# Optimization experiments

Hardware: AMD Instinct MI355X
Metric: run time of the kernel (lower is better)

## Reference

```python
import jax, jax.numpy as jnp
import numpy as np

B, N, K, V, E, H = 256, 256, 3, 32000, 256, 256
G = (3 + K) * H  # i, o, u gates + K forget gates


def setup_inputs() -> dict:
    key = jax.random.key(0)
    ks = jax.random.split(key, 6)
    node_ids = jax.random.randint(ks[0], (B, N), 0, V)
    children_raw = jax.random.randint(ks[1], (B, N, K), 0, N)
    emb = jax.random.normal(ks[2], (V, E), jnp.float32) * 0.02
    Wx_w = jax.random.normal(ks[3], (E, G), jnp.float32) * (1.0 / np.sqrt(E))
    Wx_b = jnp.zeros((G,), jnp.float32)
    Uh_w = jax.random.normal(ks[4], (K, H, G), jnp.float32) * (1.0 / np.sqrt(H))
    Uh_b = jnp.zeros((K, G), jnp.float32)
    return {"node_ids": node_ids, "children_raw": children_raw, "emb": emb,
            "Wx_w": Wx_w, "Wx_b": Wx_b, "Uh_w": Uh_w, "Uh_b": Uh_b}


def reference(node_ids, children_raw, emb, Wx_w, Wx_b, Uh_w, Uh_b):
    pos = jnp.arange(N)
    # A child slot is valid only if it points to an earlier node (topological order).
    valid = children_raw < pos[None, :, None]            # [B,N,K]
    mask = valid.astype(jnp.float32)
    cidx = jnp.where(valid, children_raw, 0)             # safe gather index

    # Input-dependent part of the gates for all nodes at once (same math as Wx(x)).
    x_all = emb[node_ids]                                # [B,N,E]
    gates_x = jnp.einsum('bne,eg->bng', x_all, Wx_w) + Wx_b  # [B,N,G]

    def step(carry, inp):
        h_buf, c_buf = carry                             # [B,N,H] each
        t, gx, idx, m = inp                              # gx:[B,G] idx,m:[B,K]
        h_child = jnp.take_along_axis(h_buf, idx[:, :, None], axis=1)  # [B,K,H]
        c_child = jnp.take_along_axis(c_buf, idx[:, :, None], axis=1)  # [B,K,H]
        # Uh[k](h_k) added only for present children (bias included per child).
        gates = gx + jnp.einsum('bkh,khg->bg', h_child * m[:, :, None], Uh_w) \
                   + m @ Uh_b                            # [B,G]
        i = jax.nn.sigmoid(gates[:, :H])
        o = jax.nn.sigmoid(gates[:, H:2 * H])
        u = jnp.tanh(gates[:, 2 * H:3 * H])
        f = jax.nn.sigmoid(gates[:, 3 * H:].reshape(B, K, H))
        c = i * u + jnp.sum(m[:, :, None] * f * c_child, axis=1)
        h = o * jnp.tanh(c)
        h_buf = jax.lax.dynamic_update_slice(h_buf, h[:, None, :], (0, t, 0))
        c_buf = jax.lax.dynamic_update_slice(c_buf, c[:, None, :], (0, t, 0))
        return (h_buf, c_buf), None

    init = (jnp.zeros((B, N, H), jnp.float32), jnp.zeros((B, N, H), jnp.float32))
    xs = (pos, gates_x.transpose(1, 0, 2), cidx.transpose(1, 0, 2), mask.transpose(1, 0, 2))
    (h_buf, _), _ = jax.lax.scan(step, init, xs)
    # Root is the last node in topological order -> encoder output [B, H].
    return h_buf[:, N - 1]
```

## Files before the change

kernel.cpp:

```cpp
#include <hip/hip_runtime.h>
#include <hip/hip_bf16.h>

#define CB 256
#define CN 256
#define CK 3
#define CE 256
#define CH 256
#define CG_ 1536
#define KTOT 1024
#define ROWS 32
#define ASTRW 1028

typedef __attribute__((ext_vector_type(8))) short short8v;
typedef __attribute__((ext_vector_type(4))) float float4v;
typedef __attribute__((ext_vector_type(4))) unsigned int uint4v;
typedef __attribute__((ext_vector_type(4))) unsigned short ushort4v;
typedef unsigned int u32;
typedef unsigned long long u64;
typedef unsigned short u16;

__device__ __forceinline__ u16 f2bfu(float v) {
    __hip_bfloat16 h = __float2bfloat16(v);
    return __builtin_bit_cast(u16, h);
}
__device__ __forceinline__ float bfu2f(u16 u) {
    __hip_bfloat16 h = __builtin_bit_cast(__hip_bfloat16, u);
    return __bfloat162float(h);
}

__global__ __launch_bounds__(256) void prep_w(
    const float* __restrict__ Wx_w, const float* __restrict__ Uh_w,
    u16* __restrict__ Whi, u16* __restrict__ Wlo)
{
    const int g    = blockIdx.x;
    const int tile = g >> 4;
    const int gl   = g & 15;
    for (int k = threadIdx.x; k < KTOT; k += 256) {
        float w = (k < CE) ? Wx_w[(size_t)k * CG_ + g]
                           : Uh_w[(size_t)(k - CE) * CG_ + g];
        u16 hi = f2bfu(w);
        u16 lo = f2bfu(w - bfu2f(hi));
        int ci = k >> 5, kr = k & 31, lq = kr >> 3, j = kr & 7;
        size_t idx = ((size_t)(tile * 32 + ci) * 64 + lq * 16 + gl) * 8 + j;
        Whi[idx] = hi;
        Wlo[idx] = lo;
    }
}

__global__ __launch_bounds__(256) void build_sched(
    const int* __restrict__ children,
    u16* __restrict__ wl,
    u32* __restrict__ lvl_start,
    u32* __restrict__ lvl_cnt,
    u32* __restrict__ nlev)
{
    __shared__ unsigned char lvl[CB][CN];
    __shared__ u32 cnt[CN];
    __shared__ u32 pos[CN];
    const int b = threadIdx.x;

    for (int t = 0; t < CN; ++t) {
        int lv = 0;
        #pragma unroll
        for (int k = 0; k < CK; ++k) {
            int raw = children[((size_t)b * CN + t) * CK + k];
            if (raw < t) { int cl = (int)lvl[b][raw] + 1; if (cl > lv) lv = cl; }
        }
        lvl[b][t] = (unsigned char)lv;
    }
    cnt[b] = 0;
    __syncthreads();
    for (int t = 0; t < CN; ++t) atomicAdd(&cnt[lvl[b][t]], 1u);
    __syncthreads();
    if (b == 0) {
        u32 acc = 0, nl = 0;
        for (int L = 0; L < CN; ++L) {
            pos[L] = acc;
            if (cnt[L]) nl = (u32)L + 1;
            acc += cnt[L];
        }
        *nlev = nl;
    }
    __syncthreads();
    lvl_cnt[b]   = cnt[b];
    lvl_start[b] = pos[b];
    __syncthreads();
    for (int t = 0; t < CN; ++t) {
        int L = lvl[b][t];
        u32 p = atomicAdd(&pos[L], 1u);
        wl[p] = (u16)((b << 8) | t);
    }
}

__global__ __launch_bounds__(512, 2) void tree_scan_lvl(
    const int* __restrict__ node_ids,
    const int* __restrict__ children,
    const float* __restrict__ emb,
    const u16* __restrict__ Whi,
    const u16* __restrict__ Wlo,
    const float* __restrict__ Wx_b,
    const float* __restrict__ Uh_b,
    u32* __restrict__ h_pk,
    float* __restrict__ c_s,
    u32* __restrict__ flags,
    const u16* __restrict__ wl,
    const u32* __restrict__ lvl_start,
    const u32* __restrict__ lvl_cnt,
    const u32* __restrict__ nlev_p,
    float* __restrict__ out)
{
    const int tid = threadIdx.x;
    const int bid = blockIdx.x;
    const int hi  = (bid & 7) >> 1;
    const int sub = ((bid >> 3) << 1) | (bid & 1);
    const int hh0 = hi * 64;

    __shared__ u32   Apk[ROWS][ASTRW];
    __shared__ int   nid[ROWS], brow[ROWS], trow[ROWS];
    __shared__ unsigned char rval[ROWS];
    __shared__ float msk[ROWS][3];
    __shared__ int   cix[ROWS][3];

    const int wv    = tid >> 6;
    const int l     = tid & 63;
    const int rg    = wv >> 2;
    const int ctq   = wv & 3;
    const int lan15 = l & 15;
    const int k8w   = (l >> 4) * 8;
    const int hcol  = hh0 + ctq * 16 + lan15;
    const int arow  = rg * 16 + lan15;

    u32 bb[6];
    #pragma unroll
    for (int q = 0; q < 6; ++q)
        bb[q] = (u32)(q * 16 + (hh0 >> 4) + ctq) * 16384u + (u32)l * 8u;

    const u32 NL = *nlev_p;

    for (u32 L = 0; L < NL; ++L) {
        const u32 lcnt   = lvl_cnt[L];
        const u32 lst    = lvl_start[L];
        const u32 nchunk = (lcnt + ROWS - 1) / ROWS;

        for (u32 ck = sub; ck < nchunk; ck += 64) {
            if (tid < ROWS) {
                u32 i = ck * ROWS + (u32)tid;
                int valid = (i < lcnt);
                u16 e = valid ? wl[lst + i] : (u16)0;
                rval[tid] = (unsigned char)valid;
                int b_ = valid ? (e >> 8) : 0;
                int t_ = valid ? (e & 0xFF) : 0;
                brow[tid] = b_;
                trow[tid] = t_;
                nid[tid]  = node_ids[(size_t)b_ * CN + t_];
            }
            if (tid < ROWS * CK) {
                int lb = tid / 3, k = tid - lb * 3;
                u32 i = ck * ROWS + (u32)lb;
                int valid = (i < lcnt);
                u16 e = valid ? wl[lst + i] : (u16)0;
                int b_ = valid ? (e >> 8) : 0;
                int t_ = valid ? (e & 0xFF) : 0;
                int raw = children[((size_t)b_ * CN + t_) * CK + k];
                int v = (raw < t_) && valid;
                msk[lb][k] = v ? 1.0f : 0.0f;
                cix[lb][k] = v ? raw : 0;
            }
            __syncthreads();

            for (int idx = tid; idx < ROWS * 64; idx += 512) {
                int row = idx >> 6, c4 = idx & 63;
                float4v v = *(const float4v*)(emb + (size_t)nid[row] * CE + c4 * 4);
                uint4v p;
                #pragma unroll
                for (int j = 0; j < 4; ++j) {
                    u16 hb = f2bfu(v[j]);
                    u16 lb = f2bfu(v[j] - bfu2f(hb));
                    p[j] = ((u32)hb << 16) | (u32)lb;
                }
                *(uint4v*)&Apk[row][c4 * 4] = p;
            }
            for (int idx = tid; idx < ROWS * CK * 128; idx += 512) {
                int r  = idx >> 7;
                int ch = idx & 127;
                int row = r / 3, k = r - row * 3;
                u64 v = 0;
                if (msk[row][k] != 0.0f) {
                    const u64* src = (const u64*)(h_pk
                        + ((size_t)cix[row][k] * CB + brow[row]) * CH + 2 * ch);
                    v = __hip_atomic_load(src, __ATOMIC_RELAXED, __HIP_MEMORY_SCOPE_AGENT);
                }
                *(u64*)&Apk[row][CE + k * CH + 2 * ch] = v;
            }
            __syncthreads();

            float4v accH[6], accL[6];
            #pragma unroll
            for (int q = 0; q < 6; ++q) {
                accH[q] = (float4v){0.f, 0.f, 0.f, 0.f};
                accL[q] = (float4v){0.f, 0.f, 0.f, 0.f};
            }
            #pragma unroll 4
            for (int ci = 0; ci < 32; ++ci) {
                uint4v a0 = *(const uint4v*)&Apk[arow][ci * 32 + k8w];
                uint4v a1 = *(const uint4v*)&Apk[arow][ci * 32 + k8w + 4];
                short8v ahi, alo;
                #pragma unroll
                for (int j = 0; j < 4; ++j) {
                    ahi[j]     = (short)(a0[j] >> 16);
                    alo[j]     = (short)(a0[j] & 0xffffu);
                    ahi[4 + j] = (short)(a1[j] >> 16);
                    alo[4 + j] = (short)(a1[j] & 0xffffu);
                }
                #pragma unroll
                for (int q = 0; q < 6; ++q) {
                    short8v bh = *(const short8v*)(Whi + bb[q] + ci * 512);
                    short8v bl = *(const short8v*)(Wlo + bb[q] + ci * 512);
                    accH[q] = __builtin_amdgcn_mfma_f32_16x16x32_bf16(ahi, bh, accH[q], 0, 0, 0);
                    accL[q] = __builtin_amdgcn_mfma_f32_16x16x32_bf16(ahi, bl, accL[q], 0, 0, 0);
                    accL[q] = __builtin_amdgcn_mfma_f32_16x16x32_bf16(alo, bh, accL[q], 0, 0, 0);
                }
            }

            #pragma unroll
            for (int r = 0; r < 4; ++r) {
                const int row = rg * 16 + (l >> 4) * 4 + r;
                if (rval[row]) {
                    const int b = brow[row], t_ = trow[row];
                    const float m0 = msk[row][0], m1 = msk[row][1], m2 = msk[row][2];
                    float g[6];
                    #pragma unroll
                    for (int q = 0; q < 6; ++q) {
                        int gc = q * CH + hcol;
                        g[q] = accH[q][r] + accL[q][r]
                             + Wx_b[gc] + m0 * Uh_b[gc] + m1 * Uh_b[CG_ + gc]
                                        + m2 * Uh_b[2 * CG_ + gc];
                    }
                    float ig = 1.0f / (1.0f + expf(-g[0]));
                    float og = 1.0f / (1.0f + expf(-g[1]));
                    float ug = tanhf(g[2]);
                    float c = ig * ug;
                    if (m0 != 0.0f) c += (1.0f / (1.0f + expf(-g[3]))) *
                        __hip_atomic_load(&c_s[((size_t)cix[row][0] * CB + b) * CH + hcol],
                                          __ATOMIC_RELAXED, __HIP_MEMORY_SCOPE_AGENT);
                    if (m1 != 0.0f) c += (1.0f / (1.0f + expf(-g[4]))) *
                        __hip_atomic_load(&c_s[((size_t)cix[row][1] * CB + b) * CH + hcol],
                                          __ATOMIC_RELAXED, __HIP_MEMORY_SCOPE_AGENT);
                    if (m2 != 0.0f) c += (1.0f / (1.0f + expf(-g[5]))) *
                        __hip_atomic_load(&c_s[((size_t)cix[row][2] * CB + b) * CH + hcol],
                                          __ATOMIC_RELAXED, __HIP_MEMORY_SCOPE_AGENT);
                    float h = og * tanhf(c);
                    const size_t hx = ((size_t)t_ * CB + b) * CH + hcol;
                    u16 hb = f2bfu(h);
                    u32 hp = ((u32)hb << 16) | (u32)f2bfu(h - bfu2f(hb));
                    __hip_atomic_store(&h_pk[hx], hp, __ATOMIC_RELAXED, __HIP_MEMORY_SCOPE_AGENT);
                    __hip_atomic_store(&c_s[hx], c, __ATOMIC_RELAXED, __HIP_MEMORY_SCOPE_AGENT);
                    if (t_ == CN - 1) out[(size_t)b * CH + hcol] = h;
                }
            }
            __syncthreads();
        }

        if (L == NL - 1) break;

        __syncthreads();
        if (tid == 0)
            __hip_atomic_store(&flags[bid * 16], L + 1,
                               __ATOMIC_RELAXED, __HIP_MEMORY_SCOPE_AGENT);
        for (;;) {
            int ok = 1;
            if (tid < 256)
                ok = (__hip_atomic_load(&flags[tid * 16], __ATOMIC_RELAXED,
                                        __HIP_MEMORY_SCOPE_AGENT) >= L + 1);
            if (__syncthreads_and(ok)) break;
            __builtin_amdgcn_s_sleep(2);
        }
    }
}

__global__ __launch_bounds__(768) void tree_step_mfma(
    const int* __restrict__ node_ids, const int* __restrict__ children,
    const float* __restrict__ emb,
    const u16* __restrict__ Whi, const u16* __restrict__ Wlo,
    const float* __restrict__ Wx_b, const float* __restrict__ Uh_b,
    u16* __restrict__ h_hi, u16* __restrict__ h_lo,
    float* __restrict__ c_s, float* __restrict__ out, const int t)
{
    const int tid = threadIdx.x;
    const int xcd  = blockIdx.x & 7;
    const int bidx = blockIdx.x >> 3;
    const int hi   = xcd * 2 + (bidx & 1);
    const int bi   = bidx >> 1;
    const int b0   = bi * 16;
    const int hh0  = hi * 16;

    __shared__ u16   Ahi[16][KTOT + 8];
    __shared__ u16   Alo[16][KTOT + 8];
    __shared__ float part[4][6][16][17];
    __shared__ int   nid[16];
    __shared__ float msk[16][3];
    __shared__ int   cix[16][3];

    const int wv    = tid >> 6;
    const int l     = tid & 63;
    const int np    = wv % 3;
    const int kq    = wv / 3;
    const int lan15 = l & 15;
    const int k8    = (l >> 4) * 8;

    if (tid < 16) nid[tid] = node_ids[(size_t)(b0 + tid) * CN + t];
    if (tid < 48) {
        int lb = tid / 3, k = tid - lb * 3;
        int raw = children[((size_t)(b0 + lb) * CN + t) * CK + k];
        int v = raw < t;
        msk[lb][k] = v ? 1.0f : 0.0f;
        cix[lb][k] = v ? raw : 0;
    }
    __syncthreads();

    for (int idx = tid; idx < 1024; idx += 768) {
        int lb = idx >> 6, c4 = idx & 63;
        float4v v = *(const float4v*)(emb + (size_t)nid[lb] * CE + c4 * 4);
        ushort4v h4, l4;
        #pragma unroll
        for (int j = 0; j < 4; ++j) {
            u16 hb = f2bfu(v[j]);
            h4[j] = hb;
            l4[j] = f2bfu(v[j] - bfu2f(hb));
        }
        *(ushort4v*)&Ahi[lb][c4 * 4] = h4;
        *(ushort4v*)&Alo[lb][c4 * 4] = l4;
    }
    for (int idx = tid; idx < 3072; idx += 768) {
        int r  = idx >> 6;
        int c  = idx & 63;
        int pl = c >> 5;
        int ch = c & 31;
        int lb = r / 3, k = r - lb * 3;
        uint4v val = (uint4v){0u, 0u, 0u, 0u};
        if (msk[lb][k] != 0.0f) {
            const u16* src = (pl ? h_lo : h_hi)
                + ((size_t)cix[lb][k] * CB + (b0 + lb)) * CH + ch * 8;
            val = *(const uint4v*)src;
        }
        u16* dst = (pl ? &Alo[lb][CE + k * CH + ch * 8]
                       : &Ahi[lb][CE + k * CH + ch * 8]);
        *(uint4v*)dst = val;
    }
    __syncthreads();

    {
        float4v acc[2][3];
        #pragma unroll
        for (int a = 0; a < 2; ++a)
            #pragma unroll
            for (int b2 = 0; b2 < 3; ++b2)
                acc[a][b2] = (float4v){0.f, 0.f, 0.f, 0.f};
        u32 fb0 = (u32)((np * 2 + 0) * 16 + hi) * 16384u + (u32)l * 8u;
        u32 fb1 = (u32)((np * 2 + 1) * 16 + hi) * 16384u + (u32)l * 8u;
        #pragma unroll
        for (int ci = 0; ci < 8; ++ci) {
            const int kb = (kq * 8 + ci) * 32 + k8;
            const u32 fo = (u32)(kq * 8 + ci) * 512u;
            short8v ahi = *(const short8v*)&Ahi[lan15][kb];
            short8v alo = *(const short8v*)&Alo[lan15][kb];
            short8v bh0 = *(const short8v*)(Whi + fb0 + fo);
            short8v bh1 = *(const short8v*)(Whi + fb1 + fo);
            short8v bl0 = *(const short8v*)(Wlo + fb0 + fo);
            short8v bl1 = *(const short8v*)(Wlo + fb1 + fo);
            acc[0][0] = __builtin_amdgcn_mfma_f32_16x16x32_bf16(ahi, bh0, acc[0][0], 0, 0, 0);
            acc[0][1] = __builtin_amdgcn_mfma_f32_16x16x32_bf16(ahi, bl0, acc[0][1], 0, 0, 0);
            acc[0][2] = __builtin_amdgcn_mfma_f32_16x16x32_bf16(alo, bh0, acc[0][2], 0, 0, 0);
            acc[1][0] = __builtin_amdgcn_mfma_f32_16x16x32_bf16(ahi, bh1, acc[1][0], 0, 0, 0);
            acc[1][1] = __builtin_amdgcn_mfma_f32_16x16x32_bf16(ahi, bl1, acc[1][1], 0, 0, 0);
            acc[1][2] = __builtin_amdgcn_mfma_f32_16x16x32_bf16(alo, bh1, acc[1][2], 0, 0, 0);
        }
        #pragma unroll
        for (int t2 = 0; t2 < 2; ++t2)
            #pragma unroll
            for (int r = 0; r < 4; ++r)
                part[kq][np * 2 + t2][(l >> 4) * 4 + r][lan15] =
                    acc[t2][0][r] + acc[t2][1][r] + acc[t2][2][r];
    }
    __syncthreads();

    if (tid < 256) {
        const int bb = tid >> 4, j2 = tid & 15;
        const int b = b0 + bb, hh = hh0 + j2;
        const float m0 = msk[bb][0], m1 = msk[bb][1], m2 = msk[bb][2];
        float g[6];
        #pragma unroll
        for (int q = 0; q < 6; ++q) {
            int gc = q * CH + hh;
            g[q] = part[0][q][bb][j2] + part[1][q][bb][j2]
                 + part[2][q][bb][j2] + part[3][q][bb][j2]
                 + Wx_b[gc] + m0 * Uh_b[gc] + m1 * Uh_b[CG_ + gc]
                            + m2 * Uh_b[2 * CG_ + gc];
        }
        float ig = 1.0f / (1.0f + expf(-g[0]));
        float og = 1.0f / (1.0f + expf(-g[1]));
        float ug = tanhf(g[2]);
        float c = ig * ug;
        if (m0 != 0.0f) c += (1.0f / (1.0f + expf(-g[3]))) * c_s[((size_t)cix[bb][0] * CB + b) * CH + hh];
        if (m1 != 0.0f) c += (1.0f / (1.0f + expf(-g[4]))) * c_s[((size_t)cix[bb][1] * CB + b) * CH + hh];
        if (m2 != 0.0f) c += (1.0f / (1.0f + expf(-g[5]))) * c_s[((size_t)cix[bb][2] * CB + b) * CH + hh];
        float h = og * tanhf(c);
        const size_t hx = ((size_t)t * CB + b) * CH + hh;
        u16 hb = f2bfu(h);
        h_hi[hx] = hb;
        h_lo[hx] = f2bfu(h - bfu2f(hb));
        c_s[hx] = c;
        if (t == CN - 1) out[(size_t)b * CH + hh] = h;
    }
}

__global__ void ws_report(float* out, int n, float val) {
    int i = blockIdx.x * blockDim.x + threadIdx.x;
    if (i < n) out[i] = val;
}

extern "C" void kernel_launch(void* const* d_in, const int* in_sizes, int n_in,
                              void* d_out, int out_size, void* d_ws, size_t ws_size,
                              hipStream_t stream) {
    float* outp = (float*)d_out;

    const int expect_sizes[7] = {65536, 196608, 8192000, 393216, 1536, 1179648, 4608};
    int bad = -1;
    if (n_in != 7) bad = 7;
    else for (int i = 0; i < 7; ++i) if (in_sizes[i] != expect_sizes[i]) { bad = i; break; }
    if (bad >= 0) {
        ws_report<<<(out_size + 255) / 256, 256, 0, stream>>>(outp, out_size, 1000.0f + bad);
        return;
    }

    const int*   node_ids = (const int*)d_in[0];
    const int*   children = (const int*)d_in[1];
    const float* emb      = (const float*)d_in[2];
    const float* Wx_w     = (const float*)d_in[3];
    const float* Wx_b     = (const float*)d_in[4];
    const float* Uh_w     = (const float*)d_in[5];
    const float* Uh_b     = (const float*)d_in[6];

    const size_t w_plane  = (size_t)CG_ * KTOT * 2;
    const size_t st_elems = (size_t)CN * CB * CH;
    const size_t flags_sz = 256 * 16 * sizeof(u32);
    const size_t wl_sz    = (size_t)CB * CN * sizeof(u16);
    const size_t lvl_sz   = 256 * sizeof(u32);

    size_t off = 0;
    const size_t o_whi = off; off += w_plane;
    const size_t o_wlo = off; off += w_plane;
    const size_t o_hpk = off; off += st_elems * 4;
    const size_t o_cs  = off; off += st_elems * 4;
    const size_t o_flg = off; off += flags_sz;
    const size_t o_wl  = off; off += wl_sz;
    const size_t o_ls  = off; off += lvl_sz;
    const size_t o_lc  = off; off += lvl_sz;
    const size_t o_nl  = off; off += 64;
    const size_t need_lvl  = off;
    const size_t need_step = 2 * w_plane + st_elems * 2 * 2 + st_elems * 4;

    if (ws_size >= need_lvl) {
        char* w = (char*)d_ws;
        u16*   Whi = (u16*)(w + o_whi);
        u16*   Wlo = (u16*)(w + o_wlo);
        u32*   hpk = (u32*)(w + o_hpk);
        float* csb = (float*)(w + o_cs);
        u32*   flg = (u32*)(w + o_flg);
        u16*   wlp = (u16*)(w + o_wl);
        u32*   lsp = (u32*)(w + o_ls);
        u32*   lcp = (u32*)(w + o_lc);
        u32*   nlp = (u32*)(w + o_nl);

        prep_w<<<dim3(CG_), dim3(256), 0, stream>>>(Wx_w, Uh_w, Whi, Wlo);
        build_sched<<<dim3(1), dim3(256), 0, stream>>>(children, wlp, lsp, lcp, nlp);
        hipMemsetAsync(flg, 0, flags_sz, stream);

        void* args[] = { (void*)&node_ids, (void*)&children, (void*)&emb,
                         (void*)&Whi, (void*)&Wlo, (void*)&Wx_b, (void*)&Uh_b,
                         (void*)&hpk, (void*)&csb, (void*)&flg,
                         (void*)&wlp, (void*)&lsp, (void*)&lcp, (void*)&nlp,
                         (void*)&outp };
        hipError_t e = hipLaunchCooperativeKernel((const void*)tree_scan_lvl,
                                                  dim3(256), dim3(512), args, 0, stream);
        if (e == hipSuccess) return;
    }
    if (ws_size >= need_step) {
        char* w = (char*)d_ws;
        u16*   Whi = (u16*)w;
        u16*   Wlo = (u16*)(w + w_plane);
        u16*   hhi = (u16*)(w + 2 * w_plane);
        u16*   hlo = (u16*)(w + 2 * w_plane + st_elems * 2);
        float* csb = (float*)(w + 2 * w_plane + 2 * st_elems * 2);

        prep_w<<<dim3(CG_), dim3(256), 0, stream>>>(Wx_w, Uh_w, Whi, Wlo);
        for (int t = 0; t < CN; ++t)
            tree_step_mfma<<<dim3(256), dim3(768), 0, stream>>>(
                node_ids, children, emb, Whi, Wlo, Wx_b, Uh_b,
                hhi, hlo, csb, outp, t);
    } else {
        ws_report<<<(out_size + 255) / 256, 256, 0, stream>>>(
            outp, out_size, (float)(ws_size >> 20));
    }
}
```

Baseline: 2.290 ms.

## Give each wave both row groups to reuse weight fragments across MFMAs

Each block now covers 128 hidden columns instead of 64: every wave owns one 16-column tile and computes both 16-row groups, so each weight fragment loaded from global memory feeds two sets of MFMAs. The column split drops from four slices to two, and the chunk stride doubles to 128 so the total work stays the same. The aim is to halve per-MFMA weight traffic. In exchange, accumulator registers double, which may reduce occupancy, and there are fewer column-parallel blocks per chunk on small tree levels.

```diff
diff --git a/kernel.cpp b/kernel.cpp
--- a/kernel.cpp
+++ b/kernel.cpp
@@ -111,9 +111,10 @@
 {
     const int tid = threadIdx.x;
     const int bid = blockIdx.x;
-    const int hi  = (bid & 7) >> 1;
-    const int sub = ((bid >> 3) << 1) | (bid & 1);
-    const int hh0 = hi * 64;
+    const int xcd   = bid & 7;
+    const int slice = xcd >> 2;
+    const int sub   = ((bid >> 3) << 2) | (bid & 3);
+    const int hh0   = slice * 128;
 
     __shared__ u32   Apk[ROWS][ASTRW];
     __shared__ int   nid[ROWS], brow[ROWS], trow[ROWS];
@@ -123,17 +124,14 @@
 
     const int wv    = tid >> 6;
     const int l     = tid & 63;
-    const int rg    = wv >> 2;
-    const int ctq   = wv & 3;
     const int lan15 = l & 15;
     const int k8w   = (l >> 4) * 8;
-    const int hcol  = hh0 + ctq * 16 + lan15;
-    const int arow  = rg * 16 + lan15;
+    const int hcol  = hh0 + wv * 16 + lan15;
 
     u32 bb[6];
     #pragma unroll
     for (int q = 0; q < 6; ++q)
-        bb[q] = (u32)(q * 16 + (hh0 >> 4) + ctq) * 16384u + (u32)l * 8u;
+        bb[q] = (u32)(q * 16 + slice * 8 + wv) * 16384u + (u32)l * 8u;
 
     const u32 NL = *nlev_p;
 
@@ -142,7 +140,7 @@
         const u32 lst    = lvl_start[L];
         const u32 nchunk = (lcnt + ROWS - 1) / ROWS;
 
-        for (u32 ck = sub; ck < nchunk; ck += 64) {
+        for (u32 ck = sub; ck < nchunk; ck += 128) {
             if (tid < ROWS) {
                 u32 i = ck * ROWS + (u32)tid;
                 int valid = (i < lcnt);
@@ -194,34 +192,44 @@
             }
             __syncthreads();
 
-            float4v accH[6], accL[6];
+            float4v accH[2][6], accL[2][6];
             #pragma unroll
-            for (int q = 0; q < 6; ++q) {
-                accH[q] = (float4v){0.f, 0.f, 0.f, 0.f};
-                accL[q] = (float4v){0.f, 0.f, 0.f, 0.f};
-            }
-            #pragma unroll 4
+            for (int rg = 0; rg < 2; ++rg)
+                #pragma unroll
+                for (int q = 0; q < 6; ++q) {
+                    accH[rg][q] = (float4v){0.f, 0.f, 0.f, 0.f};
+                    accL[rg][q] = (float4v){0.f, 0.f, 0.f, 0.f};
+                }
+            #pragma unroll 2
             for (int ci = 0; ci < 32; ++ci) {
-                uint4v a0 = *(const uint4v*)&Apk[arow][ci * 32 + k8w];
-                uint4v a1 = *(const uint4v*)&Apk[arow][ci * 32 + k8w + 4];
-                short8v ahi, alo;
+                short8v ahi[2], alo[2];
                 #pragma unroll
-                for (int j = 0; j < 4; ++j) {
-                    ahi[j]     = (short)(a0[j] >> 16);
-                    alo[j]     = (short)(a0[j] & 0xffffu);
-                    ahi[4 + j] = (short)(a1[j] >> 16);
-                    alo[4 + j] = (short)(a1[j] & 0xffffu);
+                for (int rg = 0; rg < 2; ++rg) {
+                    uint4v a0 = *(const uint4v*)&Apk[rg * 16 + lan15][ci * 32 + k8w];
+                    uint4v a1 = *(const uint4v*)&Apk[rg * 16 + lan15][ci * 32 + k8w + 4];
+                    #pragma unroll
+                    for (int j = 0; j < 4; ++j) {
+                        ahi[rg][j]     = (short)(a0[j] >> 16);
+                        alo[rg][j]     = (short)(a0[j] & 0xffffu);
+                        ahi[rg][4 + j] = (short)(a1[j] >> 16);
+                        alo[rg][4 + j] = (short)(a1[j] & 0xffffu);
+                    }
                 }
                 #pragma unroll
                 for (int q = 0; q < 6; ++q) {
                     short8v bh = *(const short8v*)(Whi + bb[q] + ci * 512);
                     short8v bl = *(const short8v*)(Wlo + bb[q] + ci * 512);
-                    accH[q] = __builtin_amdgcn_mfma_f32_16x16x32_bf16(ahi, bh, accH[q], 0, 0, 0);
-                    accL[q] = __builtin_amdgcn_mfma_f32_16x16x32_bf16(ahi, bl, accL[q], 0, 0, 0);
-                    accL[q] = __builtin_amdgcn_mfma_f32_16x16x32_bf16(alo, bh, accL[q], 0, 0, 0);
+                    #pragma unroll
+                    for (int rg = 0; rg < 2; ++rg) {
+                        accH[rg][q] = __builtin_amdgcn_mfma_f32_16x16x32_bf16(ahi[rg], bh, accH[rg][q], 0, 0, 0);
+                        accL[rg][q] = __builtin_amdgcn_mfma_f32_16x16x32_bf16(ahi[rg], bl, accL[rg][q], 0, 0, 0);
+                        accL[rg][q] = __builtin_amdgcn_mfma_f32_16x16x32_bf16(alo[rg], bh, accL[rg][q], 0, 0, 0);
+                    }
                 }
             }
 
+            #pragma unroll
+            for (int rg = 0; rg < 2; ++rg)
             #pragma unroll
             for (int r = 0; r < 4; ++r) {
                 const int row = rg * 16 + (l >> 4) * 4 + r;
@@ -232,7 +240,7 @@
                     #pragma unroll
                     for (int q = 0; q < 6; ++q) {
                         int gc = q * CH + hcol;
-                        g[q] = accH[q][r] + accL[q][r]
+                        g[q] = accH[rg][q][r] + accL[rg][q][r]
                              + Wx_b[gc] + m0 * Uh_b[gc] + m1 * Uh_b[CG_ + gc]
                                         + m2 * Uh_b[2 * CG_ + gc];
                     }
```

Measured after the change: 2.106 ms. 8.0% less time.
